# Kernel tuning notes

Hardware: AMD Instinct MI355X
Metric: run time of the kernel (lower is better)

## Reference

```python
import jax, jax.numpy as jnp
import numpy as np

B, T, C = 4, 2048, 1024
NH, HS = 16, 64            # n_head, head_size
BL, SL = 32, 16            # block_length, stride_length


def setup_inputs() -> dict:
    key = jax.random.key(0)
    ks = jax.random.split(key, 7)
    def lin(k, shape, fan_in):
        return jax.random.normal(k, shape, jnp.float32) * (1.0 / np.sqrt(fan_in))
    return {
        "x": jax.random.normal(ks[0], (B, T, C), jnp.float32),
        "W_attn": lin(ks[1], (3 * C, C), C),          # c_attn weight (bias=False)
        "W_proj": lin(ks[2], (C, C), C),              # c_proj weight
        "pos_emb": jax.random.normal(ks[3], (T, HS), jnp.float32) * 0.02,
        "W_fc": lin(ks[4], (4 * HS, BL * HS), BL * HS),   # compression c_fc
        "W_cproj": lin(ks[5], (HS, 4 * HS), 4 * HS),      # compression c_proj
        "ln_w": jnp.ones((HS,), jnp.float32),             # compression LayerNorm (bias=False)
    }


def _compress(h, pos_emb, W_fc, W_cproj, ln_w):
    # h: [B, nh, T, hs] -> [B, nh, num_blocks, hs] ; sliding windows of len BL, stride SL
    Bb, nh, Tt, hs = h.shape
    nb = max(1, (Tt - BL) // SL + 1)
    idx = jnp.arange(nb)[:, None] * SL + jnp.arange(BL)[None, :]        # [nb, BL]
    blocks = h[:, :, idx, :] + pos_emb[:BL][None, None, None, :, :]     # [B,nh,nb,BL,hs]
    flat = blocks.reshape(Bb, nh, nb, BL * hs)
    z = jax.nn.gelu(jnp.einsum('bnkf,gf->bnkg', flat, W_fc), approximate=False)
    z = jnp.einsum('bnkg,hg->bnkh', z, W_cproj)
    mu = jnp.mean(z, axis=-1, keepdims=True)
    var = jnp.var(z, axis=-1, keepdims=True)
    return (z - mu) / jnp.sqrt(var + 1e-5) * ln_w


def reference(x, W_attn, W_proj, pos_emb, W_fc, W_cproj, ln_w):
    Bb, Tt, Cc = x.shape
    qkv = x @ W_attn.T                                   # [B,T,3C]
    q, k, v = jnp.split(qkv, 3, axis=-1)
    q = q.reshape(Bb, Tt, NH, HS).transpose(0, 2, 1, 3)  # [B,nh,T,hs]
    k = k.reshape(Bb, Tt, NH, HS).transpose(0, 2, 1, 3)
    v = v.reshape(Bb, Tt, NH, HS).transpose(0, 2, 1, 3)

    # Computed (and discarded) exactly as in the torch forward.
    _kc = _compress(k, pos_emb, W_fc, W_cproj, ln_w)
    _vc = _compress(v, pos_emb, W_fc, W_cproj, ln_w)

    # Flash branch: is_causal=True -> attn_mask=None -> plain causal SDPA
    scale = 1.0 / np.sqrt(HS)
    scores = jnp.einsum('bhqd,bhkd->bhqk', q, k) * scale          # [B,nh,T,T]
    causal = jnp.tril(jnp.ones((Tt, Tt), dtype=bool))
    scores = jnp.where(causal, scores, -jnp.inf)
    att = jax.nn.softmax(scores, axis=-1)
    y = jnp.einsum('bhqk,bhkd->bhqd', att, v)                     # [B,nh,T,hs]
    y = y.transpose(0, 2, 1, 3).reshape(Bb, Tt, Cc)
    return y @ W_proj.T
```

## Files before the change

kernel.cpp:

```cpp
#include <hip/hip_runtime.h>
#include <hip/hip_bf16.h>
#include <stdint.h>


typedef __bf16 bf16x8 __attribute__((ext_vector_type(8)));
typedef float f32x4 __attribute__((ext_vector_type(4)));
typedef __hip_bfloat16 bf16;

#define B_ 4
#define T_ 2048
#define C_ 1024
#define NH_ 16
#define HS_ 64
#define NEG_BIG (-30000.0f)
#define SCALE_LOG2E 0.180336880111f

__device__ __forceinline__ bool detect_fp32(const unsigned short* px) {
  const int lane = threadIdx.x & 63;
  const unsigned short u = px[2 * lane];
  const int e = (u >> 7) & 0xff;
  const bool plausible = (e >= 117) && (e <= 137);
  return __popcll(__ballot(plausible)) < 32;
}

__device__ __forceinline__ void load_lds16(const bf16* g, bf16* l) {
  __builtin_amdgcn_global_load_lds(
      (const __attribute__((address_space(1))) void*)(uintptr_t)g,
      (__attribute__((address_space(3))) void*)(uintptr_t)l, 16, 0, 0);
}

__device__ __forceinline__ uint4 ld8f(const void* base, size_t elt) {
  const float* fp = (const float*)base + elt;
  float4 f0 = *(const float4*)(fp);
  float4 f1 = *(const float4*)(fp + 4);
  union { bf16 h[8]; uint4 u; } r;
  r.h[0] = __float2bfloat16(f0.x); r.h[1] = __float2bfloat16(f0.y);
  r.h[2] = __float2bfloat16(f0.z); r.h[3] = __float2bfloat16(f0.w);
  r.h[4] = __float2bfloat16(f1.x); r.h[5] = __float2bfloat16(f1.y);
  r.h[6] = __float2bfloat16(f1.z); r.h[7] = __float2bfloat16(f1.w);
  return r.u;
}

__global__ __launch_bounds__(256) void convert3(
    const void* __restrict__ x, const void* __restrict__ wa,
    const void* __restrict__ wp, bf16* __restrict__ xb, bf16* __restrict__ wab,
    bf16* __restrict__ wpb, const unsigned short* __restrict__ probe) {
  const bool f32 = detect_fp32(probe);
  int blk = blockIdx.x;
  const void* src;
  bf16* dst;
  if (blk < 4096) {
    src = x; dst = xb;
  } else if (blk < 4096 + 1536) {
    blk -= 4096; src = wa; dst = wab;
  } else {
    blk -= 4096 + 1536; src = wp; dst = wpb;
  }
  const size_t i = ((size_t)blk * 256 + threadIdx.x) * 8;
  if (f32)
    *(uint4*)(dst + i) = ld8f(src, i);
  else
    *(uint4*)(dst + i) = *(const uint4*)((const bf16*)src + i);
}

template <int IN_MODE, int OUT_MODE>
__global__ __launch_bounds__(256, 2) void gemm_bt(
    const void* __restrict__ A, const void* __restrict__ B, void* __restrict__ C,
    bf16* __restrict__ k_ws, bf16* __restrict__ v_ws,
    const unsigned short* __restrict__ in_probe,
    const unsigned short* __restrict__ out_probe, int M, int N, int K) {
  __shared__ bf16 As[128 * 32];
  __shared__ bf16 Bs[128 * 32];

  const bool f32b = in_probe ? detect_fp32(in_probe) : false;
  const bool f32a = (IN_MODE == 0) && f32b;
  const bool f32out =
      (OUT_MODE == 0) && (out_probe ? detect_fp32(out_probe) : false);

  const int tid = threadIdx.x;
  const int lane = tid & 63;
  const int wid = tid >> 6;
  const int quad = lane >> 4;
  const int col = lane & 15;
  const int m0 = blockIdx.y * 128;
  const int n0 = blockIdx.x * 128;
  const int wm = (wid >> 1) * 64;
  const int wn = (wid & 1) * 64;
  const bool vsec = (OUT_MODE == 1) && ((n0 >> 10) == 2);

  const size_t arow = (size_t)(m0 + (tid >> 2));
  const size_t brow = (size_t)(n0 + (tid >> 2));
  const int chunk = (tid & 3) * 8;

  f32x4 acc[4][4] = {};

  for (int k0 = 0; k0 < K; k0 += 32) {
    const bf16* ap0;
    const bf16* ap1;
    if (IN_MODE == 0) {
      ap0 = (const bf16*)A + arow * K + chunk + k0;
      ap1 = (const bf16*)A + (arow + 64) * K + chunk + k0;
    } else {
      const int b = m0 >> 11;
      const int tloc = (m0 & 2047) + (tid >> 2);
      const size_t aoff = ((((size_t)b * NH_) + (k0 >> 6)) * T_ + tloc) * HS_ +
                          (k0 & 32) + chunk;
      ap0 = (const bf16*)A + aoff;
      ap1 = (const bf16*)A + aoff + (size_t)64 * HS_;
    }

    uint4 a0, a1, b0, b1;
    if (f32a) {
      a0 = ld8f(A, arow * K + chunk + k0);
      a1 = ld8f(A, (arow + 64) * K + chunk + k0);
    }
    if (f32b) {
      b0 = ld8f(B, brow * K + chunk + k0);
      b1 = ld8f(B, (brow + 64) * K + chunk + k0);
    }

    __syncthreads();
    if (f32a) {
      *(uint4*)(As + tid * 8) = a0;
      *(uint4*)(As + 2048 + tid * 8) = a1;
    } else {
      load_lds16(ap0, As + tid * 8);
      load_lds16(ap1, As + 2048 + tid * 8);
    }
    if (f32b) {
      *(uint4*)(Bs + tid * 8) = b0;
      *(uint4*)(Bs + 2048 + tid * 8) = b1;
    } else {
      load_lds16((const bf16*)B + brow * K + chunk + k0, Bs + tid * 8);
      load_lds16((const bf16*)B + (brow + 64) * K + chunk + k0,
                 Bs + 2048 + tid * 8);
    }
    __syncthreads();

    bf16x8 af[4], bfr[4];
#pragma unroll
    for (int t = 0; t < 4; ++t) {
      af[t] = *(const bf16x8*)(As + (wm + t * 16 + col) * 32 + quad * 8);
      bfr[t] = *(const bf16x8*)(Bs + (wn + t * 16 + col) * 32 + quad * 8);
    }
    if (vsec) {
#pragma unroll
      for (int tm = 0; tm < 4; ++tm)
#pragma unroll
        for (int tn = 0; tn < 4; ++tn)
          acc[tm][tn] = __builtin_amdgcn_mfma_f32_16x16x32_bf16(
              bfr[tn], af[tm], acc[tm][tn], 0, 0, 0);
    } else {
#pragma unroll
      for (int tm = 0; tm < 4; ++tm)
#pragma unroll
        for (int tn = 0; tn < 4; ++tn)
          acc[tm][tn] = __builtin_amdgcn_mfma_f32_16x16x32_bf16(
              af[tm], bfr[tn], acc[tm][tn], 0, 0, 0);
    }
  }

  if (OUT_MODE == 0) {
#pragma unroll
    for (int tm = 0; tm < 4; ++tm) {
      const int mrow = m0 + wm + tm * 16 + quad * 4;
#pragma unroll
      for (int tn = 0; tn < 4; ++tn) {
        const int ncol = n0 + wn + tn * 16 + col;
#pragma unroll
        for (int r = 0; r < 4; ++r) {
          if (f32out)
            ((float*)C)[(size_t)(mrow + r) * N + ncol] = acc[tm][tn][r];
          else
            ((bf16*)C)[(size_t)(mrow + r) * N + ncol] =
                __float2bfloat16(acc[tm][tn][r]);
        }
      }
    }
  } else if (vsec) {
    const int b = m0 >> 11;
#pragma unroll
    for (int tm = 0; tm < 4; ++tm) {
      const int tloc = (m0 & 2047) + wm + tm * 16 + col;
#pragma unroll
      for (int tn = 0; tn < 4; ++tn) {
        const int vch = (n0 & (C_ - 1)) + wn + tn * 16 + quad * 4;
#pragma unroll
        for (int r = 0; r < 4; ++r) {
          const int h = (vch + r) >> 6, d = (vch + r) & 63;
          v_ws[(((size_t)b * NH_ + h) * HS_ + d) * T_ + tloc] =
              __float2bfloat16(acc[tm][tn][r]);
        }
      }
    }
  } else {
    const int sect = n0 >> 10;
    bf16* dst = (sect == 0) ? (bf16*)C : k_ws;
#pragma unroll
    for (int tm = 0; tm < 4; ++tm) {
      const int mrow = m0 + wm + tm * 16 + quad * 4;
#pragma unroll
      for (int tn = 0; tn < 4; ++tn) {
        const int c = (n0 + wn + tn * 16 + col) & (C_ - 1);
        const int h = c >> 6, d = c & 63;
#pragma unroll
        for (int r = 0; r < 4; ++r) {
          const int t = (mrow + r) & (T_ - 1);
          const int b = (mrow + r) >> 11;
          dst[(((size_t)b * NH_ + h) * T_ + t) * HS_ + d] =
              __float2bfloat16(acc[tm][tn][r]);
        }
      }
    }
  }
}

__global__ __launch_bounds__(256, 2) void attn(
    bf16* qy, const bf16* __restrict__ kws, const bf16* __restrict__ vws) {
  __shared__ bf16 Ks[64 * 72];
  __shared__ bf16 Vs[64 * 72];
  __shared__ bf16 Ps[4][32 * 72];

  const int tid = threadIdx.x;
  const int lane = tid & 63;
  const int w = tid >> 6;
  const int quad = lane >> 4;
  const int col = lane & 15;
  const int gx = (int)gridDim.x;
  const int hx = gx >> 1;
  const int x = (int)blockIdx.x;
  const int qb = (x < hx) ? (gx - 1 - x) : (x - hx);
  const int bh = blockIdx.y;
  const size_t head_off = (size_t)bh * T_ * HS_;

  const int qrow = qb * 128 + w * 32 + col;
  const bf16* qp = qy + head_off + (size_t)qrow * HS_ + quad * 8;
  bf16x8 qf0a = *(const bf16x8*)(qp);
  bf16x8 qf1a = *(const bf16x8*)(qp + 32);
  bf16x8 qf0b = *(const bf16x8*)(qp + 16 * HS_);
  bf16x8 qf1b = *(const bf16x8*)(qp + 16 * HS_ + 32);
#pragma unroll
  for (int j = 0; j < 8; ++j) {
    qf0a[j] = (__bf16)((float)qf0a[j] * SCALE_LOG2E);
    qf1a[j] = (__bf16)((float)qf1a[j] * SCALE_LOG2E);
    qf0b[j] = (__bf16)((float)qf0b[j] * SCALE_LOG2E);
    qf1b[j] = (__bf16)((float)qf1b[j] * SCALE_LOG2E);
  }

  bf16x8 onesf;
#pragma unroll
  for (int j = 0; j < 8; ++j) onesf[j] = (__bf16)1.0f;

  f32x4 oa[4] = {}, ob[4] = {};
  f32x4 lacca = {}, laccb = {};

  bf16* pw = &Ps[w][0];
  const int ntiles = 2 * (qb + 1);

  const int srow = tid >> 3, sch = tid & 7;
  const bf16* kg = kws + head_off + (size_t)srow * HS_ + sch * 8;
  const bf16* vg = vws + ((size_t)bh * HS_ + srow) * T_ + sch * 8;
  bf16* kl0 = Ks + srow * 72 + sch * 8;
  bf16* kl1 = Ks + (srow + 32) * 72 + sch * 8;
  bf16* vl0 = Vs + srow * 72 + sch * 8;
  bf16* vl1 = Vs + (srow + 32) * 72 + sch * 8;

  uint4 kr0 = *(const uint4*)(kg);
  uint4 kr1 = *(const uint4*)(kg + (size_t)32 * HS_);
  uint4 vr0 = *(const uint4*)(vg);
  uint4 vr1 = *(const uint4*)(vg + (size_t)32 * T_);

  const int qga = qb * 128 + w * 32 + col;
  const int diag_start = 2 * qb;

  for (int kt = 0; kt < ntiles; ++kt) {
    const int k0 = kt * 64;
    __syncthreads();
    *(uint4*)kl0 = kr0;
    *(uint4*)kl1 = kr1;
    *(uint4*)vl0 = vr0;
    *(uint4*)vl1 = vr1;
    __syncthreads();
    if (kt + 1 < ntiles) {
      kg += (size_t)64 * HS_;
      vg += 64;
      kr0 = *(const uint4*)(kg);
      kr1 = *(const uint4*)(kg + (size_t)32 * HS_);
      vr0 = *(const uint4*)(vg);
      vr1 = *(const uint4*)(vg + (size_t)32 * T_);
    }

    f32x4 sa[4], sb[4];
#pragma unroll
    for (int nt = 0; nt < 4; ++nt) {
      const bf16* kp = Ks + (nt * 16 + col) * 72 + quad * 8;
      bf16x8 kf0 = *(const bf16x8*)(kp);
      bf16x8 kf1 = *(const bf16x8*)(kp + 32);
      f32x4 a = {-32.0f, -32.0f, -32.0f, -32.0f};
      a = __builtin_amdgcn_mfma_f32_16x16x32_bf16(kf0, qf0a, a, 0, 0, 0);
      a = __builtin_amdgcn_mfma_f32_16x16x32_bf16(kf1, qf1a, a, 0, 0, 0);
      sa[nt] = a;
      f32x4 b = {-32.0f, -32.0f, -32.0f, -32.0f};
      b = __builtin_amdgcn_mfma_f32_16x16x32_bf16(kf0, qf0b, b, 0, 0, 0);
      b = __builtin_amdgcn_mfma_f32_16x16x32_bf16(kf1, qf1b, b, 0, 0, 0);
      sb[nt] = b;
    }

    if (kt >= diag_start) {
#pragma unroll
      for (int nt = 0; nt < 4; ++nt) {
        const int key = k0 + nt * 16 + quad * 4;
#pragma unroll
        for (int r = 0; r < 4; ++r) {
          if (key + r > qga) sa[nt][r] = NEG_BIG;
          if (key + r > qga + 16) sb[nt][r] = NEG_BIG;
        }
      }
    }

#pragma unroll
    for (int nt = 0; nt < 4; ++nt) {
      union { ushort u[4]; uint2 v; } pa, pb;
#pragma unroll
      for (int r = 0; r < 4; ++r) {
        pa.u[r] = __bfloat16_as_ushort(__float2bfloat16(exp2f(sa[nt][r])));
        pb.u[r] = __bfloat16_as_ushort(__float2bfloat16(exp2f(sb[nt][r])));
      }
      *(uint2*)(pw + col * 72 + nt * 16 + quad * 4) = pa.v;
      *(uint2*)(pw + (col + 16) * 72 + nt * 16 + quad * 4) = pb.v;
    }

    __asm__ __volatile__("s_waitcnt lgkmcnt(0)" ::: "memory");

#pragma unroll
    for (int half = 0; half < 2; ++half) {
      bf16x8 pfa = *(const bf16x8*)(pw + col * 72 + half * 32 + quad * 8);
      bf16x8 pfb = *(const bf16x8*)(pw + (col + 16) * 72 + half * 32 + quad * 8);
      lacca = __builtin_amdgcn_mfma_f32_16x16x32_bf16(pfa, onesf, lacca, 0, 0, 0);
      laccb = __builtin_amdgcn_mfma_f32_16x16x32_bf16(pfb, onesf, laccb, 0, 0, 0);
#pragma unroll
      for (int dt = 0; dt < 4; ++dt) {
        bf16x8 vf = *(const bf16x8*)(Vs + (dt * 16 + col) * 72 + half * 32 +
                                     quad * 8);
        oa[dt] = __builtin_amdgcn_mfma_f32_16x16x32_bf16(pfa, vf, oa[dt], 0, 0, 0);
        ob[dt] = __builtin_amdgcn_mfma_f32_16x16x32_bf16(pfb, vf, ob[dt], 0, 0, 0);
      }
    }
  }

  float inva[4], invb[4];
#pragma unroll
  for (int r = 0; r < 4; ++r) {
    inva[r] = 1.0f / lacca[r];
    invb[r] = 1.0f / laccb[r];
  }
#pragma unroll
  for (int dt = 0; dt < 4; ++dt)
#pragma unroll
    for (int r = 0; r < 4; ++r) {
      const int qa = qb * 128 + w * 32 + quad * 4 + r;
      qy[head_off + (size_t)qa * HS_ + dt * 16 + col] =
          __float2bfloat16(oa[dt][r] * inva[r]);
      qy[head_off + (size_t)(qa + 16) * HS_ + dt * 16 + col] =
          __float2bfloat16(ob[dt][r] * invb[r]);
    }
}

extern "C" void kernel_launch(void* const* d_in, const int* in_sizes, int n_in,
                              void* d_out, int out_size, void* d_ws, size_t ws_size,
                              hipStream_t stream) {
  const void* x = d_in[0];
  const void* W_attn = d_in[1];
  const void* W_proj = d_in[2];
  const unsigned short* probe = (const unsigned short*)d_in[0];

  const size_t qkv_elems = (size_t)B_ * NH_ * T_ * HS_;
  const size_t xe = (size_t)B_ * T_ * C_;
  const size_t wae = (size_t)3 * C_ * C_;
  const size_t wpe = (size_t)C_ * C_;

  bf16* q_ws = (bf16*)d_ws;
  bf16* k_ws = q_ws + qkv_elems;
  bf16* v_ws = k_ws + qkv_elems;
  bf16* x_bf = v_ws + qkv_elems;
  bf16* wa_bf = x_bf + xe;
  bf16* wp_bf = wa_bf + wae;
  const size_t need = (3 * qkv_elems + xe + wae + wpe) * sizeof(bf16);

  const int M = B_ * T_;

  if (ws_size >= need) {
    convert3<<<6144, 256, 0, stream>>>(x, W_attn, W_proj, x_bf, wa_bf, wp_bf,
                                       probe);
    gemm_bt<0, 1><<<dim3(3 * C_ / 128, M / 128), 256, 0, stream>>>(
        x_bf, wa_bf, q_ws, k_ws, v_ws, nullptr, nullptr, M, 3 * C_, C_);
    attn<<<dim3(T_ / 128, B_ * NH_), 256, 0, stream>>>(q_ws, k_ws, v_ws);
    gemm_bt<1, 0><<<dim3(C_ / 128, M / 128), 256, 0, stream>>>(
        q_ws, wp_bf, d_out, nullptr, nullptr, nullptr, probe, M, C_, C_);
  } else {
    gemm_bt<0, 1><<<dim3(3 * C_ / 128, M / 128), 256, 0, stream>>>(
        x, W_attn, q_ws, k_ws, v_ws, probe, nullptr, M, 3 * C_, C_);
    attn<<<dim3(T_ / 128, B_ * NH_), 256, 0, stream>>>(q_ws, k_ws, v_ws);
    gemm_bt<1, 0><<<dim3(C_ / 128, M / 128), 256, 0, stream>>>(
        q_ws, W_proj, d_out, nullptr, nullptr, probe, probe, M, C_, C_);
  }
}
```

Measured before the change: 321.1 us.

## Split long causal query blocks across two workgroups with combine kernel

Query blocks 8-15 of the causal attention are split into two key-range chunks of up to 16 tiles each, so that no workgroup processes more than 16 key tiles. The unnormalized fp32 partial outputs and row sums go to workspace and a new combine kernel adds and normalizes them. The goal is better load balance across the grid, which grows from 16 to 24 blocks per head. The cost is an extra kernel launch, fp32 partial-output traffic, and an added workspace requirement; the split path runs only when the workspace is large enough.

```diff
diff --git a/kernel.cpp b/kernel.cpp
--- a/kernel.cpp
+++ b/kernel.cpp
@@ -215,8 +215,10 @@
   }
 }
 
+template <int SPLIT>
 __global__ __launch_bounds__(256, 2) void attn(
-    bf16* qy, const bf16* __restrict__ kws, const bf16* __restrict__ vws) {
+    bf16* qy, const bf16* __restrict__ kws, const bf16* __restrict__ vws,
+    float* __restrict__ po, float* __restrict__ pl) {
   __shared__ bf16 Ks[64 * 72];
   __shared__ bf16 Vs[64 * 72];
   __shared__ bf16 Ps[4][32 * 72];
@@ -226,12 +228,29 @@
   const int w = tid >> 6;
   const int quad = lane >> 4;
   const int col = lane & 15;
-  const int gx = (int)gridDim.x;
-  const int hx = gx >> 1;
   const int x = (int)blockIdx.x;
-  const int qb = (x < hx) ? (gx - 1 - x) : (x - hx);
+
+  int qb, ck;
+  if (SPLIT) {
+    const unsigned long long lo = 0xC4D5E6F7FEDCBA98ULL;
+    const unsigned int hi = 0xB3A29180u;
+    const unsigned int cmask = 0x00AAAA00u;
+    qb = (x < 16) ? (int)((lo >> (4 * x)) & 15)
+                  : (int)((hi >> (4 * (x - 16))) & 15);
+    ck = (int)((cmask >> x) & 1);
+  } else {
+    const int gx = (int)gridDim.x;
+    const int hx = gx >> 1;
+    qb = (x < hx) ? (gx - 1 - x) : (x - hx);
+    ck = 0;
+  }
+
   const int bh = blockIdx.y;
   const size_t head_off = (size_t)bh * T_ * HS_;
+
+  const int ntall = 2 * (qb + 1);
+  const int kt0 = SPLIT ? ck * 16 : 0;
+  const int ntiles = SPLIT ? min(ntall - kt0, 16) : ntall;
 
   const int qrow = qb * 128 + w * 32 + col;
   const bf16* qp = qy + head_off + (size_t)qrow * HS_ + quad * 8;
@@ -255,11 +274,10 @@
   f32x4 lacca = {}, laccb = {};
 
   bf16* pw = &Ps[w][0];
-  const int ntiles = 2 * (qb + 1);
 
   const int srow = tid >> 3, sch = tid & 7;
-  const bf16* kg = kws + head_off + (size_t)srow * HS_ + sch * 8;
-  const bf16* vg = vws + ((size_t)bh * HS_ + srow) * T_ + sch * 8;
+  const bf16* kg = kws + head_off + (size_t)(kt0 * 64 + srow) * HS_ + sch * 8;
+  const bf16* vg = vws + ((size_t)bh * HS_ + srow) * T_ + kt0 * 64 + sch * 8;
   bf16* kl0 = Ks + srow * 72 + sch * 8;
   bf16* kl1 = Ks + (srow + 32) * 72 + sch * 8;
   bf16* vl0 = Vs + srow * 72 + sch * 8;
@@ -274,7 +292,8 @@
   const int diag_start = 2 * qb;
 
   for (int kt = 0; kt < ntiles; ++kt) {
-    const int k0 = kt * 64;
+    const int ktg = kt0 + kt;
+    const int k0 = ktg * 64;
     __syncthreads();
     *(uint4*)kl0 = kr0;
     *(uint4*)kl1 = kr1;
@@ -306,7 +325,7 @@
       sb[nt] = b;
     }
 
-    if (kt >= diag_start) {
+    if (ktg >= diag_start) {
 #pragma unroll
       for (int nt = 0; nt < 4; ++nt) {
         const int key = k0 + nt * 16 + quad * 4;
@@ -348,22 +367,70 @@
     }
   }
 
-  float inva[4], invb[4];
-#pragma unroll
-  for (int r = 0; r < 4; ++r) {
-    inva[r] = 1.0f / lacca[r];
-    invb[r] = 1.0f / laccb[r];
-  }
-#pragma unroll
-  for (int dt = 0; dt < 4; ++dt)
+  const bool dosplit = SPLIT && (qb >= 8);
+  if (!dosplit) {
+    float inva[4], invb[4];
 #pragma unroll
     for (int r = 0; r < 4; ++r) {
-      const int qa = qb * 128 + w * 32 + quad * 4 + r;
-      qy[head_off + (size_t)qa * HS_ + dt * 16 + col] =
-          __float2bfloat16(oa[dt][r] * inva[r]);
-      qy[head_off + (size_t)(qa + 16) * HS_ + dt * 16 + col] =
-          __float2bfloat16(ob[dt][r] * invb[r]);
-    }
+      inva[r] = 1.0f / lacca[r];
+      invb[r] = 1.0f / laccb[r];
+    }
+#pragma unroll
+    for (int dt = 0; dt < 4; ++dt)
+#pragma unroll
+      for (int r = 0; r < 4; ++r) {
+        const int qa = qb * 128 + w * 32 + quad * 4 + r;
+        qy[head_off + (size_t)qa * HS_ + dt * 16 + col] =
+            __float2bfloat16(oa[dt][r] * inva[r]);
+        qy[head_off + (size_t)(qa + 16) * HS_ + dt * 16 + col] =
+            __float2bfloat16(ob[dt][r] * invb[r]);
+      }
+  } else {
+    const int slot = ((qb - 8) * 64 + bh) * 2 + ck;
+    float* o = po + (size_t)slot * (128 * 64);
+#pragma unroll
+    for (int dt = 0; dt < 4; ++dt)
+#pragma unroll
+      for (int r = 0; r < 4; ++r) {
+        const int qa = w * 32 + quad * 4 + r;
+        o[(size_t)qa * 64 + dt * 16 + col] = oa[dt][r];
+        o[(size_t)(qa + 16) * 64 + dt * 16 + col] = ob[dt][r];
+      }
+    if (col == 0) {
+      float* lp = pl + (size_t)slot * 128;
+#pragma unroll
+      for (int r = 0; r < 4; ++r) {
+        lp[w * 32 + quad * 4 + r] = lacca[r];
+        lp[w * 32 + 16 + quad * 4 + r] = laccb[r];
+      }
+    }
+  }
+}
+
+__global__ __launch_bounds__(256) void attn_combine(
+    bf16* __restrict__ qy, const float* __restrict__ po,
+    const float* __restrict__ pl) {
+  const int qb = 8 + (int)blockIdx.x;
+  const int bh = (int)blockIdx.y;
+  const int pair = ((qb - 8) * 64 + bh) * 2;
+  const float* o0 = po + (size_t)pair * (128 * 64);
+  const float* o1 = o0 + 128 * 64;
+  const float* l0 = pl + (size_t)pair * 128;
+  const float* l1 = l0 + 128;
+  const int q = threadIdx.x >> 1;
+  const int d0 = (threadIdx.x & 1) * 32;
+  const float inv = 1.0f / (l0[q] + l1[q]);
+  const size_t base =
+      (size_t)bh * T_ * HS_ + (size_t)(qb * 128 + q) * HS_ + d0;
+  const size_t ob = (size_t)q * 64 + d0;
+#pragma unroll
+  for (int j0 = 0; j0 < 32; j0 += 8) {
+    union { bf16 h[8]; uint4 u; } out;
+#pragma unroll
+    for (int j = 0; j < 8; ++j)
+      out.h[j] = __float2bfloat16((o0[ob + j0 + j] + o1[ob + j0 + j]) * inv);
+    *(uint4*)(qy + base + j0) = out.u;
+  }
 }
 
 extern "C" void kernel_launch(void* const* d_in, const int* in_sizes, int n_in,
@@ -387,6 +454,11 @@
   bf16* wp_bf = wa_bf + wae;
   const size_t need = (3 * qkv_elems + xe + wae + wpe) * sizeof(bf16);
 
+  float* po = (float*)(wp_bf + wpe);
+  float* pl = po + (size_t)1024 * 128 * 64;
+  const size_t need2 =
+      need + ((size_t)1024 * 128 * 64 + (size_t)1024 * 128) * sizeof(float);
+
   const int M = B_ * T_;
 
   if (ws_size >= need) {
@@ -394,13 +466,20 @@
                                        probe);
     gemm_bt<0, 1><<<dim3(3 * C_ / 128, M / 128), 256, 0, stream>>>(
         x_bf, wa_bf, q_ws, k_ws, v_ws, nullptr, nullptr, M, 3 * C_, C_);
-    attn<<<dim3(T_ / 128, B_ * NH_), 256, 0, stream>>>(q_ws, k_ws, v_ws);
+    if (ws_size >= need2) {
+      attn<1><<<dim3(24, B_ * NH_), 256, 0, stream>>>(q_ws, k_ws, v_ws, po, pl);
+      attn_combine<<<dim3(8, B_ * NH_), 256, 0, stream>>>(q_ws, po, pl);
+    } else {
+      attn<0><<<dim3(T_ / 128, B_ * NH_), 256, 0, stream>>>(q_ws, k_ws, v_ws,
+                                                            nullptr, nullptr);
+    }
     gemm_bt<1, 0><<<dim3(C_ / 128, M / 128), 256, 0, stream>>>(
         q_ws, wp_bf, d_out, nullptr, nullptr, nullptr, probe, M, C_, C_);
   } else {
     gemm_bt<0, 1><<<dim3(3 * C_ / 128, M / 128), 256, 0, stream>>>(
         x, W_attn, q_ws, k_ws, v_ws, probe, nullptr, M, 3 * C_, C_);
-    attn<<<dim3(T_ / 128, B_ * NH_), 256, 0, stream>>>(q_ws, k_ws, v_ws);
+    attn<0><<<dim3(T_ / 128, B_ * NH_), 256, 0, stream>>>(q_ws, k_ws, v_ws,
+                                                          nullptr, nullptr);
     gemm_bt<1, 0><<<dim3(C_ / 128, M / 128), 256, 0, stream>>>(
         q_ws, W_proj, d_out, nullptr, nullptr, probe, probe, M, C_, C_);
   }
```

New measurement: 300.3 us. 1.07x faster.
